# Performance work log

Hardware: AMD Instinct MI355X
Metric: run time of the kernel (lower is better)

## Reference

```python
import jax, jax.numpy as jnp
import numpy as np
import math

B, S, D, H = 1, 4096, 1024, 16
HD = D // H  # head_dim = 64


def setup_inputs() -> dict:
    key = jax.random.key(0)
    ks = jax.random.split(key, 6)
    x = jax.random.normal(ks[0], (B, S, D), dtype=jnp.float32)
    # Llama-style rotary frequencies: theta = 10000^{-2i/head_dim}
    inv_freq = 1.0 / (10000.0 ** (jnp.arange(0, HD, 2, dtype=jnp.float32) / HD))  # (HD/2,)
    t = jnp.arange(S, dtype=jnp.float32)
    freqs = jnp.outer(t, inv_freq)  # (S, HD/2)
    cos = jnp.cos(freqs)
    sin = jnp.sin(freqs)
    # additive causal mask (S, S): 0 on/below diagonal, -inf above
    mask = jnp.where(jnp.tril(jnp.ones((S, S), dtype=bool)), 0.0, -jnp.inf).astype(jnp.float32)
    scale = 1.0 / math.sqrt(D)
    wq = jax.random.normal(ks[1], (D, D), dtype=jnp.float32) * scale
    wk = jax.random.normal(ks[2], (D, D), dtype=jnp.float32) * scale
    wv = jax.random.normal(ks[3], (D, D), dtype=jnp.float32) * scale
    wo = jax.random.normal(ks[4], (D, D), dtype=jnp.float32) * scale
    return {"x": x, "cos": cos, "sin": sin, "mask": mask,
            "wq": wq, "wk": wk, "wv": wv, "wo": wo, "start_pos": 0}


def _rope(t, cos, sin):
    # t: (b, s, h, hd); cos/sin: (s, hd/2). Interleaved-pair complex rotation.
    b, s, h, hd = t.shape
    tr = t.reshape(b, s, h, hd // 2, 2)
    te, to = tr[..., 0], tr[..., 1]
    c = cos[None, :, None, :]
    sn = sin[None, :, None, :]
    oe = te * c - to * sn
    oo = te * sn + to * c
    return jnp.stack([oe, oo], axis=-1).reshape(b, s, h, hd)


def reference(x, cos, sin, mask, wq, wk, wv, wo, start_pos):
    b, s, d = x.shape
    h, hd = H, HD
    # Linear layers: y = x @ W.T (torch nn.Linear convention, W is (out,in))
    xq = (x @ wq.T).reshape(b, s, h, hd)
    xk = (x @ wk.T).reshape(b, s, h, hd)
    xv = (x @ wv.T).reshape(b, s, h, hd)
    xq = _rope(xq, cos, sin)
    xk = _rope(xk, cos, sin)
    # (b, h, s, hd)
    xq = xq.transpose(0, 2, 1, 3)
    xk = xk.transpose(0, 2, 1, 3)
    xv = xv.transpose(0, 2, 1, 3)
    scores = jnp.einsum('bhqd,bhkd->bhqk', xq, xk) / math.sqrt(hd)
    scores = scores + mask[None, None, :, :]
    attn = jax.nn.softmax(scores.astype(jnp.float32), axis=-1).astype(xq.dtype)
    out = jnp.einsum('bhqk,bhkd->bhqd', attn, xv)
    out = out.transpose(0, 2, 1, 3).reshape(b, s, d)
    return out @ wo.T
```

## Files before the change

kernel.cpp:

```cpp
#include <hip/hip_runtime.h>
#include <hip/hip_bf16.h>
#include <math.h>

typedef __bf16 bf16;
typedef __bf16 bf16x4 __attribute__((ext_vector_type(4)));
typedef __bf16 bf16x8 __attribute__((ext_vector_type(8)));
typedef float floatx4 __attribute__((ext_vector_type(4)));
typedef short short4v __attribute__((ext_vector_type(4)));

#define S_LEN 4096
#define DM 1024
#define NH 16
#define HD 64

#define GM 4096
#define GN 1024
#define GK 1024
#define LDST 72
#define FST 68

#define GLDS16(gp, lp) __builtin_amdgcn_global_load_lds( \
    (const __attribute__((address_space(1))) void*)(gp), \
    (__attribute__((address_space(3))) void*)(lp), 16, 0, 0)

__device__ __forceinline__ bf16x8 cvt8(float4 a, float4 b) {
    return (bf16x8){ (bf16)a.x, (bf16)a.y, (bf16)a.z, (bf16)a.w,
                     (bf16)b.x, (bf16)b.y, (bf16)b.z, (bf16)b.w };
}

__global__ void cvt_bf16(const float* __restrict__ x,  const float* __restrict__ wq,
                         const float* __restrict__ wk, const float* __restrict__ wv,
                         const float* __restrict__ wo, bf16* __restrict__ dst)
{
    size_t i4 = ((size_t)blockIdx.x * 256 + threadIdx.x) * 4;
    const float* src; size_t off;
    const size_t M1 = (size_t)1 << 20;
    if      (i4 < 4 * M1) { src = x;  off = i4;          }
    else if (i4 < 5 * M1) { src = wq; off = i4 - 4 * M1; }
    else if (i4 < 6 * M1) { src = wk; off = i4 - 5 * M1; }
    else if (i4 < 7 * M1) { src = wv; off = i4 - 6 * M1; }
    else                  { src = wo; off = i4 - 7 * M1; }
    float4 v = *(const float4*)(src + off);
    bf16x4 o = { (bf16)v.x, (bf16)v.y, (bf16)v.z, (bf16)v.w };
    *(bf16x4*)(&dst[i4]) = o;
}

__launch_bounds__(256)
__global__ void gemm_qkv(const bf16* __restrict__ A,
                         const bf16* __restrict__ B0, const bf16* __restrict__ B1,
                         const bf16* __restrict__ B2,
                         const float* __restrict__ cosp, const float* __restrict__ sinp,
                         bf16* __restrict__ Qw, bf16* __restrict__ Kw,
                         bf16* __restrict__ VTw)
{
    const int bz = blockIdx.z;
    const bf16* __restrict__ B = (bz == 0) ? B0 : (bz == 1 ? B1 : B2);

    const int tid  = threadIdx.x;
    const int wave = tid >> 6;
    const int lane = tid & 63;
    const int wm   = (wave >> 1) * 64;
    const int wn   = (wave & 1) * 64;
    const int lrow = lane >> 4;
    const int lcol = lane & 15;

    const int m0 = blockIdx.y * 128;
    const int n0 = blockIdx.x * 128;

    __shared__ __align__(16) bf16 As[128 * 64];
    __shared__ __align__(16) bf16 Bs[128 * 64];

    floatx4 acc[4][4];
    #pragma unroll
    for (int i = 0; i < 4; i++)
        #pragma unroll
        for (int j = 0; j < 4; j++) acc[i][j] = (floatx4){0.f, 0.f, 0.f, 0.f};

    const bf16* ga0 = A + (size_t)(m0 + wave * 32 + (lane >> 3)) * GK + (lane & 7) * 8;
    const bf16* gb0 = B + (size_t)(n0 + wave * 32 + (lane >> 3)) * GK + (lane & 7) * 8;
    bf16* la = &As[(wave * 32) * 64];
    bf16* lb = &Bs[(wave * 32) * 64];

    for (int kt = 0; kt < GK; kt += 64) {
        #pragma unroll
        for (int i = 0; i < 4; i++) {
            GLDS16(ga0 + kt + (size_t)i * 8 * GK, la + i * 8 * 64);
            GLDS16(gb0 + kt + (size_t)i * 8 * GK, lb + i * 8 * 64);
        }
        __syncthreads();
        #pragma unroll
        for (int ks = 0; ks < 2; ks++) {
            bf16x8 af[4], bfr[4];
            #pragma unroll
            for (int t = 0; t < 4; t++) {
                af[t]  = *(const bf16x8*)(&As[(wm + t * 16 + lcol) * 64 + ks * 32 + lrow * 8]);
                bfr[t] = *(const bf16x8*)(&Bs[(wn + t * 16 + lcol) * 64 + ks * 32 + lrow * 8]);
            }
            #pragma unroll
            for (int mt = 0; mt < 4; mt++)
                #pragma unroll
                for (int nt = 0; nt < 4; nt++)
                    acc[mt][nt] = __builtin_amdgcn_mfma_f32_16x16x32_bf16(af[mt], bfr[nt], acc[mt][nt], 0, 0, 0);
        }
        __syncthreads();
    }

    if (bz < 2) {
        bf16* __restrict__ C = bz ? Kw : Qw;
        const bool odd = (lcol & 1);
        #pragma unroll
        for (int mt = 0; mt < 4; mt++)
            #pragma unroll
            for (int nt = 0; nt < 4; nt++) {
                int i = (nt * 16 + lcol) >> 1;
                #pragma unroll
                for (int r = 0; r < 4; r++) {
                    float v  = acc[mt][nt][r];
                    float pv = __shfl_xor(v, 1, 64);
                    int s = m0 + wm + mt * 16 + lrow * 4 + r;
                    float c  = cosp[s * 32 + i];
                    float sn = sinp[s * 32 + i];
                    float ov = odd ? (pv * sn + v * c) : (v * c - pv * sn);
                    C[(size_t)s * GN + n0 + wn + nt * 16 + lcol] = (bf16)ov;
                }
            }
    } else {
        #pragma unroll
        for (int mt = 0; mt < 4; mt++)
            #pragma unroll
            for (int nt = 0; nt < 4; nt++) {
                int col = n0 + wn + nt * 16 + lcol;
                int s   = m0 + wm + mt * 16 + lrow * 4;
                bf16x4 ov = { (bf16)acc[mt][nt][0], (bf16)acc[mt][nt][1],
                              (bf16)acc[mt][nt][2], (bf16)acc[mt][nt][3] };
                *(bf16x4*)(&VTw[(size_t)col * S_LEN + s]) = ov;
            }
    }
}

__launch_bounds__(256, 4)
__global__ void flash_attn(const bf16* __restrict__ Q, const bf16* __restrict__ K,
                           const bf16* __restrict__ VT,
                           float* __restrict__ O0, float* __restrict__ O1,
                           float* __restrict__ L0, float* __restrict__ L1)
{
    const int pi   = blockIdx.x >> 1;
    const int p    = blockIdx.x & 1;
    const int h    = blockIdx.y;
    const int tid  = threadIdx.x;
    const int wave = tid >> 6;
    const int lane = tid & 63;
    const int lrow = lane >> 4;
    const int lcol = lane & 15;

    const int qtA = pi;
    const int qtB = 63 - pi;

    float* __restrict__ Op = p ? O1 : O0;
    float* __restrict__ Lp = p ? L1 : L0;

    __shared__ __align__(16) bf16 Ks[2][64 * FST];
    __shared__ __align__(16) bf16 Vs[2][64 * FST];

    const float sc2 = 0.125f * 1.44269504088896340736f;

    const int q0A = qtA * 64 + wave * 16;
    const int q0B = qtB * 64 + wave * 16;

    const bf16* qpA = Q + (size_t)(q0A + lcol) * DM + h * HD;
    const bf16* qpB = Q + (size_t)(q0B + lcol) * DM + h * HD;
    bf16x8 qfA[2], qfB[2];
    qfA[0] = *(const bf16x8*)(qpA + 0 + lrow * 8);
    qfA[1] = *(const bf16x8*)(qpA + 32 + lrow * 8);
    qfB[0] = *(const bf16x8*)(qpB + 0 + lrow * 8);
    qfB[1] = *(const bf16x8*)(qpB + 32 + lrow * 8);

    float lA = 0.f, lB = 0.f;
    floatx4 oaccA[4], oaccB[4];
    #pragma unroll
    for (int nt = 0; nt < 4; nt++) {
        oaccA[nt] = (floatx4){0.f, 0.f, 0.f, 0.f};
        oaccB[nt] = (floatx4){0.f, 0.f, 0.f, 0.f};
    }

    const int  srow = tid >> 3;
    const int  sch  = (tid & 7) * 8;
    const bf16* kp  = K  + (size_t)srow * DM + h * HD + sch;
    const bf16* vp  = VT + (size_t)(h * HD + srow) * S_LEN + sch;
    const int  wof  = srow * FST + sch;

    {
        size_t ko = (size_t)p * 64 * DM;
        size_t vo = (size_t)p * 64;
        uint4 a = *(const uint4*)(kp + ko);
        uint4 b = *(const uint4*)(kp + ko + (size_t)32 * DM);
        uint4 c = *(const uint4*)(vp + vo);
        uint4 d = *(const uint4*)(vp + vo + (size_t)32 * S_LEN);
        *(uint4*)(&Ks[0][wof])            = a;
        *(uint4*)(&Ks[0][wof + 32 * FST]) = b;
        *(uint4*)(&Vs[0][wof])            = c;
        *(uint4*)(&Vs[0][wof + 32 * FST]) = d;
    }
    __syncthreads();

    uint4 kr0, kr1, vr0, vr1;
    for (int t = p; t <= qtB; t += 2) {
        const int  cur  = ((t - p) >> 1) & 1;
        const bool more = (t + 2 <= qtB);
        const bool actA = (t <= qtA);

        if (more) {
            size_t ko = (size_t)(t + 2) * 64 * DM;
            size_t vo = (size_t)(t + 2) * 64;
            kr0 = *(const uint4*)(kp + ko);
            kr1 = *(const uint4*)(kp + ko + (size_t)32 * DM);
            vr0 = *(const uint4*)(vp + vo);
            vr1 = *(const uint4*)(vp + vo + (size_t)32 * S_LEN);
        }

        short4v pbA[4], pbB[4];
        const bool diagA = (t == qtA);
        const bool diagB = (t == qtB);
        #pragma unroll
        for (int nt = 0; nt < 4; nt++) {
            floatx4 zB = (floatx4){0.f, 0.f, 0.f, 0.f};
            floatx4 zA = (floatx4){0.f, 0.f, 0.f, 0.f};
            #pragma unroll
            for (int ks = 0; ks < 2; ks++) {
                bf16x8 kf = *(const bf16x8*)(&Ks[cur][(nt * 16 + lcol) * FST + ks * 32 + lrow * 8]);
                zB = __builtin_amdgcn_mfma_f32_16x16x32_bf16(kf, qfB[ks], zB, 0, 0, 0);
                if (actA)
                    zA = __builtin_amdgcn_mfma_f32_16x16x32_bf16(kf, qfA[ks], zA, 0, 0, 0);
            }
            if (diagB) {
                #pragma unroll
                for (int r = 0; r < 4; r++) {
                    int kg = t * 64 + nt * 16 + lrow * 4 + r;
                    float pr = exp2f(zB[r] * sc2);
                    if (kg > q0B + lcol) pr = 0.f;
                    zB[r] = pr; lB += pr;
                }
            } else {
                #pragma unroll
                for (int r = 0; r < 4; r++) {
                    float pr = exp2f(zB[r] * sc2);
                    zB[r] = pr; lB += pr;
                }
            }
            bf16x4 pvB = { (bf16)zB[0], (bf16)zB[1], (bf16)zB[2], (bf16)zB[3] };
            pbB[nt] = __builtin_bit_cast(short4v, pvB);
            if (actA) {
                if (diagA) {
                    #pragma unroll
                    for (int r = 0; r < 4; r++) {
                        int kg = t * 64 + nt * 16 + lrow * 4 + r;
                        float pr = exp2f(zA[r] * sc2);
                        if (kg > q0A + lcol) pr = 0.f;
                        zA[r] = pr; lA += pr;
                    }
                } else {
                    #pragma unroll
                    for (int r = 0; r < 4; r++) {
                        float pr = exp2f(zA[r] * sc2);
                        zA[r] = pr; lA += pr;
                    }
                }
                bf16x4 pvA = { (bf16)zA[0], (bf16)zA[1], (bf16)zA[2], (bf16)zA[3] };
                pbA[nt] = __builtin_bit_cast(short4v, pvA);
            }
        }

        #pragma unroll
        for (int nt = 0; nt < 4; nt++)
            #pragma unroll
            for (int kt = 0; kt < 4; kt++) {
                bf16x4 va = *(const bf16x4*)(&Vs[cur][(nt * 16 + lcol) * FST + kt * 16 + lrow * 4]);
                short4v vas = __builtin_bit_cast(short4v, va);
                oaccB[nt] = __builtin_amdgcn_mfma_f32_16x16x16bf16_1k(vas, pbB[kt], oaccB[nt], 0, 0, 0);
                if (actA)
                    oaccA[nt] = __builtin_amdgcn_mfma_f32_16x16x16bf16_1k(vas, pbA[kt], oaccA[nt], 0, 0, 0);
            }

        if (more) {
            int nxt = cur ^ 1;
            *(uint4*)(&Ks[nxt][wof])            = kr0;
            *(uint4*)(&Ks[nxt][wof + 32 * FST]) = kr1;
            *(uint4*)(&Vs[nxt][wof])            = vr0;
            *(uint4*)(&Vs[nxt][wof + 32 * FST]) = vr1;
        }
        __syncthreads();
    }

    lA += __shfl_xor(lA, 16, 64);
    lA += __shfl_xor(lA, 32, 64);
    lB += __shfl_xor(lB, 16, 64);
    lB += __shfl_xor(lB, 32, 64);
    if (lrow == 0) {
        Lp[h * S_LEN + q0A + lcol] = lA;
        Lp[h * S_LEN + q0B + lcol] = lB;
    }
    #pragma unroll
    for (int nt = 0; nt < 4; nt++) {
        *(floatx4*)(&Op[(size_t)(q0A + lcol) * DM + h * HD + nt * 16 + lrow * 4]) = oaccA[nt];
        *(floatx4*)(&Op[(size_t)(q0B + lcol) * DM + h * HD + nt * 16 + lrow * 4]) = oaccB[nt];
    }
}

__launch_bounds__(256)
__global__ void gemm_out(const float* __restrict__ O0, const float* __restrict__ O1,
                         const float* __restrict__ L0, const float* __restrict__ L1,
                         const bf16* __restrict__ wo, float* __restrict__ out)
{
    const int tid  = threadIdx.x;
    const int wave = tid >> 6;
    const int lane = tid & 63;
    const int wm   = (wave >> 1) * 64;
    const int wn   = (wave & 1) * 64;
    const int lrow = lane >> 4;
    const int lcol = lane & 15;

    const int m0 = blockIdx.y * 128;
    const int n0 = blockIdx.x * 128;

    __shared__ __align__(16) bf16 As[128 * LDST];
    __shared__ __align__(16) bf16 Bs[128 * LDST];

    floatx4 acc[4][4];
    #pragma unroll
    for (int i = 0; i < 4; i++)
        #pragma unroll
        for (int j = 0; j < 4; j++) acc[i][j] = (floatx4){0.f, 0.f, 0.f, 0.f};

    for (int kt = 0; kt < GK; kt += 64) {
        #pragma unroll
        for (int i = 0; i < 4; i++) {
            int idx = i * 256 + tid;
            int row = idx >> 3;
            int ch  = (idx & 7) * 8;
            int s   = m0 + row;
            int hh  = (kt + ch) >> 6;
            float rl = 1.f / (L0[hh * S_LEN + s] + L1[hh * S_LEN + s]);
            const float* a0p = &O0[(size_t)s * GK + kt + ch];
            const float* a1p = &O1[(size_t)s * GK + kt + ch];
            float4 a0 = *(const float4*)(a0p), a1 = *(const float4*)(a0p + 4);
            float4 b0 = *(const float4*)(a1p), b1 = *(const float4*)(a1p + 4);
            bf16x8 av = { (bf16)((a0.x + b0.x) * rl), (bf16)((a0.y + b0.y) * rl),
                          (bf16)((a0.z + b0.z) * rl), (bf16)((a0.w + b0.w) * rl),
                          (bf16)((a1.x + b1.x) * rl), (bf16)((a1.y + b1.y) * rl),
                          (bf16)((a1.z + b1.z) * rl), (bf16)((a1.w + b1.w) * rl) };
            *(bf16x8*)(&As[row * LDST + ch]) = av;
            *(uint4*)(&Bs[row * LDST + ch]) =
                *(const uint4*)(&wo[(size_t)(n0 + row) * GK + kt + ch]);
        }
        __syncthreads();
        #pragma unroll
        for (int ks = 0; ks < 2; ks++) {
            bf16x8 af[4], bfr[4];
            #pragma unroll
            for (int t = 0; t < 4; t++) {
                af[t]  = *(const bf16x8*)(&As[(wm + t * 16 + lcol) * LDST + ks * 32 + lrow * 8]);
                bfr[t] = *(const bf16x8*)(&Bs[(wn + t * 16 + lcol) * LDST + ks * 32 + lrow * 8]);
            }
            #pragma unroll
            for (int mt = 0; mt < 4; mt++)
                #pragma unroll
                for (int nt = 0; nt < 4; nt++)
                    acc[mt][nt] = __builtin_amdgcn_mfma_f32_16x16x32_bf16(af[mt], bfr[nt], acc[mt][nt], 0, 0, 0);
        }
        __syncthreads();
    }

    #pragma unroll
    for (int mt = 0; mt < 4; mt++)
        #pragma unroll
        for (int nt = 0; nt < 4; nt++)
            #pragma unroll
            for (int r = 0; r < 4; r++) {
                int row = m0 + wm + mt * 16 + lrow * 4 + r;
                int col = n0 + wn + nt * 16 + lcol;
                out[(size_t)row * GN + col] = acc[mt][nt][r];
            }
}

extern "C" void kernel_launch(void* const* d_in, const int* in_sizes, int n_in,
                              void* d_out, int out_size, void* d_ws, size_t ws_size,
                              hipStream_t stream) {
    const float* x    = (const float*)d_in[0];
    const float* cosp = (const float*)d_in[1];
    const float* sinp = (const float*)d_in[2];
    const float* wq   = (const float*)d_in[4];
    const float* wk   = (const float*)d_in[5];
    const float* wv   = (const float*)d_in[6];
    const float* wo   = (const float*)d_in[7];
    float* out = (float*)d_out;

    const size_t SD = (size_t)S_LEN * DM;
    const size_t DD = (size_t)DM * DM;
    bf16* xb  = (bf16*)d_ws;
    bf16* wqb = xb + SD;
    bf16* wkb = wqb + DD;
    bf16* wvb = wkb + DD;
    bf16* wob = wvb + DD;
    bf16* Qw  = wob + DD;
    bf16* Kw  = Qw + SD;
    bf16* VTw = Kw + SD;
    float* O0f = (float*)(VTw + SD);
    float* O1f = O0f + SD;
    float* L0f = O1f + SD;
    float* L1f = L0f + (size_t)S_LEN * NH;

    cvt_bf16<<<8192, 256, 0, stream>>>(x, wq, wk, wv, wo, xb);
    gemm_qkv<<<dim3(GN / 128, GM / 128, 3), 256, 0, stream>>>(
        xb, wqb, wkb, wvb, cosp, sinp, Qw, Kw, VTw);
    flash_attn<<<dim3(64, NH), 256, 0, stream>>>(Qw, Kw, VTw, O0f, O1f, L0f, L1f);
    gemm_out<<<dim3(GN / 128, GM / 128, 1), 256, 0, stream>>>(
        O0f, O1f, L0f, L1f, wob, out);
}
```

Baseline: 315.3 us.

## Split attention combine into separate kernel and use direct-to-LDS loads in output GEMM

The flash-attention partial outputs are now merged and normalized in a standalone elementwise kernel that writes a bf16 activation buffer. The output projection GEMM then streams bf16 A and W tiles into shared memory with global_load_lds, drops the padded LDS stride, and uses 64x128 tiles to launch more blocks. This removes redundant fp32 reads and conversion work from the GEMM's inner loop, at the cost of an extra launch, an extra round trip through global memory, and possible LDS bank conflicts from the unpadded layout.

```diff
diff --git a/kernel.cpp b/kernel.cpp
--- a/kernel.cpp
+++ b/kernel.cpp
@@ -16,17 +16,11 @@
 #define GM 4096
 #define GN 1024
 #define GK 1024
-#define LDST 72
 #define FST 68
 
 #define GLDS16(gp, lp) __builtin_amdgcn_global_load_lds( \
     (const __attribute__((address_space(1))) void*)(gp), \
     (__attribute__((address_space(3))) void*)(lp), 16, 0, 0)
-
-__device__ __forceinline__ bf16x8 cvt8(float4 a, float4 b) {
-    return (bf16x8){ (bf16)a.x, (bf16)a.y, (bf16)a.z, (bf16)a.w,
-                     (bf16)b.x, (bf16)b.y, (bf16)b.z, (bf16)b.w };
-}
 
 __global__ void cvt_bf16(const float* __restrict__ x,  const float* __restrict__ wq,
                          const float* __restrict__ wk, const float* __restrict__ wv,
@@ -306,63 +300,70 @@
     }
 }
 
+__global__ void combine_kernel(const float* __restrict__ O0, const float* __restrict__ O1,
+                               const float* __restrict__ L0, const float* __restrict__ L1,
+                               bf16* __restrict__ Aw)
+{
+    int i4 = (blockIdx.x * 256 + threadIdx.x) * 4;
+    int q = i4 >> 10;
+    int c = i4 & 1023;
+    int h = c >> 6;
+    float rl = 1.f / (L0[h * S_LEN + q] + L1[h * S_LEN + q]);
+    float4 a = *(const float4*)(O0 + i4);
+    float4 b = *(const float4*)(O1 + i4);
+    bf16x4 o = { (bf16)((a.x + b.x) * rl), (bf16)((a.y + b.y) * rl),
+                 (bf16)((a.z + b.z) * rl), (bf16)((a.w + b.w) * rl) };
+    *(bf16x4*)(&Aw[i4]) = o;
+}
+
 __launch_bounds__(256)
-__global__ void gemm_out(const float* __restrict__ O0, const float* __restrict__ O1,
-                         const float* __restrict__ L0, const float* __restrict__ L1,
-                         const bf16* __restrict__ wo, float* __restrict__ out)
+__global__ void gemm_out(const bf16* __restrict__ A, const bf16* __restrict__ B,
+                         float* __restrict__ out)
 {
     const int tid  = threadIdx.x;
     const int wave = tid >> 6;
     const int lane = tid & 63;
-    const int wm   = (wave >> 1) * 64;
+    const int wm   = (wave >> 1) * 32;
     const int wn   = (wave & 1) * 64;
     const int lrow = lane >> 4;
     const int lcol = lane & 15;
 
-    const int m0 = blockIdx.y * 128;
+    const int m0 = blockIdx.y * 64;
     const int n0 = blockIdx.x * 128;
 
-    __shared__ __align__(16) bf16 As[128 * LDST];
-    __shared__ __align__(16) bf16 Bs[128 * LDST];
-
-    floatx4 acc[4][4];
+    __shared__ __align__(16) bf16 As[64 * 64];
+    __shared__ __align__(16) bf16 Bs[128 * 64];
+
+    floatx4 acc[2][4];
     #pragma unroll
-    for (int i = 0; i < 4; i++)
+    for (int i = 0; i < 2; i++)
         #pragma unroll
         for (int j = 0; j < 4; j++) acc[i][j] = (floatx4){0.f, 0.f, 0.f, 0.f};
 
+    const bf16* ga0 = A + (size_t)(m0 + wave * 16 + (lane >> 3)) * GK + (lane & 7) * 8;
+    const bf16* gb0 = B + (size_t)(n0 + wave * 32 + (lane >> 3)) * GK + (lane & 7) * 8;
+    bf16* la = &As[(wave * 16) * 64];
+    bf16* lb = &Bs[(wave * 32) * 64];
+
     for (int kt = 0; kt < GK; kt += 64) {
         #pragma unroll
-        for (int i = 0; i < 4; i++) {
-            int idx = i * 256 + tid;
-            int row = idx >> 3;
-            int ch  = (idx & 7) * 8;
-            int s   = m0 + row;
-            int hh  = (kt + ch) >> 6;
-            float rl = 1.f / (L0[hh * S_LEN + s] + L1[hh * S_LEN + s]);
-            const float* a0p = &O0[(size_t)s * GK + kt + ch];
-            const float* a1p = &O1[(size_t)s * GK + kt + ch];
-            float4 a0 = *(const float4*)(a0p), a1 = *(const float4*)(a0p + 4);
-            float4 b0 = *(const float4*)(a1p), b1 = *(const float4*)(a1p + 4);
-            bf16x8 av = { (bf16)((a0.x + b0.x) * rl), (bf16)((a0.y + b0.y) * rl),
-                          (bf16)((a0.z + b0.z) * rl), (bf16)((a0.w + b0.w) * rl),
-                          (bf16)((a1.x + b1.x) * rl), (bf16)((a1.y + b1.y) * rl),
-                          (bf16)((a1.z + b1.z) * rl), (bf16)((a1.w + b1.w) * rl) };
-            *(bf16x8*)(&As[row * LDST + ch]) = av;
-            *(uint4*)(&Bs[row * LDST + ch]) =
-                *(const uint4*)(&wo[(size_t)(n0 + row) * GK + kt + ch]);
-        }
+        for (int i = 0; i < 2; i++)
+            GLDS16(ga0 + kt + (size_t)i * 8 * GK, la + i * 8 * 64);
+        #pragma unroll
+        for (int i = 0; i < 4; i++)
+            GLDS16(gb0 + kt + (size_t)i * 8 * GK, lb + i * 8 * 64);
         __syncthreads();
         #pragma unroll
         for (int ks = 0; ks < 2; ks++) {
-            bf16x8 af[4], bfr[4];
-            #pragma unroll
-            for (int t = 0; t < 4; t++) {
-                af[t]  = *(const bf16x8*)(&As[(wm + t * 16 + lcol) * LDST + ks * 32 + lrow * 8]);
-                bfr[t] = *(const bf16x8*)(&Bs[(wn + t * 16 + lcol) * LDST + ks * 32 + lrow * 8]);
-            }
-            #pragma unroll
-            for (int mt = 0; mt < 4; mt++)
+            bf16x8 af[2], bfr[4];
+            #pragma unroll
+            for (int t = 0; t < 2; t++)
+                af[t]  = *(const bf16x8*)(&As[(wm + t * 16 + lcol) * 64 + ks * 32 + lrow * 8]);
+            #pragma unroll
+            for (int t = 0; t < 4; t++)
+                bfr[t] = *(const bf16x8*)(&Bs[(wn + t * 16 + lcol) * 64 + ks * 32 + lrow * 8]);
+            #pragma unroll
+            for (int mt = 0; mt < 2; mt++)
                 #pragma unroll
                 for (int nt = 0; nt < 4; nt++)
                     acc[mt][nt] = __builtin_amdgcn_mfma_f32_16x16x32_bf16(af[mt], bfr[nt], acc[mt][nt], 0, 0, 0);
@@ -371,7 +372,7 @@
     }
 
     #pragma unroll
-    for (int mt = 0; mt < 4; mt++)
+    for (int mt = 0; mt < 2; mt++)
         #pragma unroll
         for (int nt = 0; nt < 4; nt++)
             #pragma unroll
@@ -404,7 +405,8 @@
     bf16* Qw  = wob + DD;
     bf16* Kw  = Qw + SD;
     bf16* VTw = Kw + SD;
-    float* O0f = (float*)(VTw + SD);
+    bf16* Aw  = VTw + SD;
+    float* O0f = (float*)(Aw + SD);
     float* O1f = O0f + SD;
     float* L0f = O1f + SD;
     float* L1f = L0f + (size_t)S_LEN * NH;
@@ -413,6 +415,6 @@
     gemm_qkv<<<dim3(GN / 128, GM / 128, 3), 256, 0, stream>>>(
         xb, wqb, wkb, wvb, cosp, sinp, Qw, Kw, VTw);
     flash_attn<<<dim3(64, NH), 256, 0, stream>>>(Qw, Kw, VTw, O0f, O1f, L0f, L1f);
-    gemm_out<<<dim3(GN / 128, GM / 128, 1), 256, 0, stream>>>(
-        O0f, O1f, L0f, L1f, wob, out);
-}
+    combine_kernel<<<S_LEN * DM / 1024, 256, 0, stream>>>(O0f, O1f, L0f, L1f, Aw);
+    gemm_out<<<dim3(GN / 128, GM / 64), 256, 0, stream>>>(Aw, wob, out);
+}
```

Measured after the change: 297.2 us. 1.06x faster.
